# Kernel tuning notes

Hardware: AMD Instinct MI355X
Metric: run time of the kernel (lower is better)

Reference implementation:

```python
import jax, jax.numpy as jnp
import numpy as np

KERNEL_SIZE = 5
SIGMA = 2.0
HALF_K = KERNEL_SIZE // 2


def _gaussian_kernel():
    # torch: arange(-k//2+1, k//2+1) with python floor div -> [-2,...,2] for k=5
    ax = jnp.arange(-(KERNEL_SIZE // 2), KERNEL_SIZE // 2 + 1, dtype=jnp.float32)
    xx, yy = jnp.meshgrid(ax, ax, indexing='ij')
    k = jnp.exp(-(xx ** 2 + yy ** 2) / (2.0 * SIGMA ** 2))
    return k / k.sum()  # [5,5]


def setup_inputs() -> dict:
    key = jax.random.key(0)
    k1, k2 = jax.random.split(key)
    feature_map = jax.random.normal(k1, (512, 256, 256), dtype=jnp.float32)
    keypoints = jax.random.randint(k2, (4096, 2), 0, 256, dtype=jnp.int64)
    return {"feature_map": feature_map, "keypoints": keypoints}


def reference(feature_map, keypoints):
    C, H, W = feature_map.shape
    kern = _gaussian_kernel().astype(feature_map.dtype)  # [5,5]
    x = jnp.clip(keypoints[:, 0].astype(jnp.int32), HALF_K, W - HALF_K - 1)  # [N]
    y = jnp.clip(keypoints[:, 1].astype(jnp.int32), HALF_K, H - HALF_K - 1)  # [N]

    def pool_one(xi, yi):
        patch = jax.lax.dynamic_slice(
            feature_map, (0, yi - HALF_K, xi - HALF_K), (C, KERNEL_SIZE, KERNEL_SIZE)
        )  # [C,5,5]
        return jnp.einsum('chw,hw->c', patch, kern)  # [C]

    return jax.vmap(pool_one)(x, y)  # [N,C]
```

## Files before the change

kernel.cpp:

```cpp
#include <hip/hip_runtime.h>


#define NC  512
#define NH  256
#define NW  256
#define NKP 4096

#define NSTRIP 16
#define SLICE_ROWS 20
#define STR 260

#define WS_LIST_OFF_I 8192

__global__ __launch_bounds__(256) void bucket_kernel(
    const int* __restrict__ kp, unsigned* __restrict__ ws_i, int n_kp)
{
    __shared__ int hist[NSTRIP];
    __shared__ int base[NSTRIP];
    const int t = threadIdx.x;
    const int i = blockIdx.x * 256 + t;

    if (t < NSTRIP) hist[t] = 0;
    __syncthreads();

    int q = 0, lr = 0;
    unsigned pk = 0;
    const bool valid = (i < n_kp);
    if (valid) {
        int x = kp[2 * i + 0];
        int y = kp[2 * i + 1];
        x = min(max(x, 2), NW - 3);
        y = min(max(y, 2), NH - 3);
        q  = y >> 4;
        lr = atomicAdd(&hist[q], 1);
        pk = (unsigned)i | ((unsigned)x << 12) | ((unsigned)y << 20);
    }
    __syncthreads();

    if (t < NSTRIP) base[t] = atomicAdd((int*)&ws_i[t], hist[t]);
    __syncthreads();

    if (valid)
        ws_i[WS_LIST_OFF_I + q * NKP + base[q] + lr] = pk;
}

__global__ __launch_bounds__(256) void pool_kernel(
    const float* __restrict__ fm, const unsigned* __restrict__ ws_i,
    float* __restrict__ out)
{
    __shared__ float plane[SLICE_ROWS * STR];

    const int b     = blockIdx.x;
    const int x7    = b & 7;
    const int inner = b >> 3;
    const int hi    = inner >> 8;
    const int rem   = inner & 255;
    const int q     = rem >> 4;
    const int lane  = rem & 15;
    const int chunk = (hi << 3) | x7;
    const int c     = (chunk << 4) | lane;

    const int t = threadIdx.x;
    const int ybase = (q << 4) - 2;

    const float4* src = (const float4*)(fm + ((size_t)c << 16));
#pragma unroll
    for (int it = 0; it < 5; ++it) {
        const int i = t + it * 256;
        const int row  = i >> 6;
        const int col4 = i & 63;
        const int gr   = ybase + row;
        if ((unsigned)gr < 256u) {
            float4 v = src[(gr << 6) + col4];
            *(float4*)&plane[row * STR + (col4 << 2)] = v;
        }
    }
    __syncthreads();

    const float e1 = 0.8824969025845955f;
    const float e2 = 0.6065306597126334f;
    const float s  = 2.0f * (e1 + e2) + 1.0f;
    const float inv_s2 = 1.0f / (s * s);
    const float g[5] = {e2, e1, 1.0f, e1, e2};
    float gy[5];
#pragma unroll
    for (int i = 0; i < 5; i++) gy[i] = g[i] * inv_s2;

    const int cnt = (int)ws_i[q];
    const unsigned* list = ws_i + WS_LIST_OFF_I + q * NKP;

    for (int e = t; e < cnt; e += 256) {
        const unsigned pk = list[e];
        const int n  = (int)(pk & 0xFFFu);
        const int xc = (int)((pk >> 12) & 0xFFu);
        const int yc = (int)((pk >> 20) & 0xFFu);

        const int x0 = xc - 2;
        const int r  = x0 & 3;
        const int xa = x0 - r;
        float wx[8];
#pragma unroll
        for (int i = 0; i < 8; i++)
            wx[i] = (i >= r && i < r + 5) ? g[i - r] : 0.0f;

        const int lr0 = yc - (q << 4);
        float acc = 0.0f;
#pragma unroll
        for (int dy = 0; dy < 5; dy++) {
            const float* rowp = &plane[(lr0 + dy) * STR + xa];
            float4 a = *(const float4*)rowp;
            float4 b4 = *(const float4*)(rowp + 4);
            acc += gy[dy] * (a.x * wx[0] + a.y * wx[1] + a.z * wx[2] + a.w * wx[3]
                           + b4.x * wx[4] + b4.y * wx[5] + b4.z * wx[6] + b4.w * wx[7]);
        }
        out[(size_t)n * NC + c] = acc;
    }
}

__global__ __launch_bounds__(256) void gpool_direct_kernel(
    const float* __restrict__ fm, const int* __restrict__ kp,
    float* __restrict__ out)
{
    const int n = blockIdx.x;
    const int t = threadIdx.x;

    int x = kp[2 * n + 0];
    int y = kp[2 * n + 1];
    x = min(max(x, 2), NW - 3);
    y = min(max(y, 2), NH - 3);

    const float e1 = 0.8824969025845955f;
    const float e2 = 0.6065306597126334f;
    const float s  = 2.0f * (e1 + e2) + 1.0f;
    const float inv_s2 = 1.0f / (s * s);
    float g[5] = {e2, e1, 1.0f, e1, e2};
    float gy[5];
#pragma unroll
    for (int i = 0; i < 5; i++) gy[i] = g[i] * inv_s2;

    const int x0 = x - 2;
    const int r  = x0 & 3;
    const int xa = x0 - r;
    float wx[8];
#pragma unroll
    for (int i = 0; i < 8; i++)
        wx[i] = (i >= r && i < r + 5) ? g[i - r] : 0.0f;

    const float* base0 = fm + ((size_t)t * NH + (y - 2)) * NW + xa;
    const float* base1 = fm + ((size_t)(t + 256) * NH + (y - 2)) * NW + xa;

    float acc0 = 0.0f, acc1 = 0.0f;
#pragma unroll
    for (int dy = 0; dy < 5; dy++) {
        const float4* p0 = (const float4*)(base0 + dy * NW);
        const float4* p1 = (const float4*)(base1 + dy * NW);
        float4 a0 = p0[0], b0 = p0[1], a1 = p1[0], b1 = p1[1];
        acc0 += gy[dy] * (a0.x * wx[0] + a0.y * wx[1] + a0.z * wx[2] + a0.w * wx[3]
                        + b0.x * wx[4] + b0.y * wx[5] + b0.z * wx[6] + b0.w * wx[7]);
        acc1 += gy[dy] * (a1.x * wx[0] + a1.y * wx[1] + a1.z * wx[2] + a1.w * wx[3]
                        + b1.x * wx[4] + b1.y * wx[5] + b1.z * wx[6] + b1.w * wx[7]);
    }

    out[(size_t)n * NC + t]       = acc0;
    out[(size_t)n * NC + t + 256] = acc1;
}

extern "C" void kernel_launch(void* const* d_in, const int* in_sizes, int n_in,
                              void* d_out, int out_size, void* d_ws, size_t ws_size,
                              hipStream_t stream)
{
    const float* fm  = (const float*)d_in[0];
    const int*   kp  = (const int*)d_in[1];
    float*       out = (float*)d_out;
    const int n_kp   = in_sizes[1] / 2;

    const size_t need = (WS_LIST_OFF_I + (size_t)NSTRIP * NKP) * sizeof(unsigned);
    if (ws_size >= need && n_kp == NKP) {
        unsigned* ws_i = (unsigned*)d_ws;

        hipMemsetAsync(d_ws, 0, NSTRIP * sizeof(unsigned), stream);

        bucket_kernel<<<(NKP + 255) / 256, 256, 0, stream>>>(kp, ws_i, n_kp);

        pool_kernel<<<NC * NSTRIP, 256, 0, stream>>>(fm, ws_i, out);
    } else {
        gpool_direct_kernel<<<n_kp, 256, 0, stream>>>(fm, kp, out);
    }
}
```

Before: 203.8 us.

## Use single-block bucketing and direct global-to-LDS loads for strip staging

The bucketing pass now runs in one 1024-thread block that writes counts directly. This removes the memset and the global atomics used to compute per-block bases. The pool kernel stages each feature-map strip into shared memory with global_load_lds (buffer-to-LDS DMA) instead of loading through registers, and it moves the count load and weight setup before the barrier so they overlap the transfer. The trade-offs are that bucketing is serialized onto a single CU and the code now depends on an AMD-specific builtin with 16-byte width support.

After: 200.6 us. About the same (-1.6%).

```diff
diff --git a/kernel.cpp b/kernel.cpp
--- a/kernel.cpp
+++ b/kernel.cpp
@@ -12,36 +12,41 @@
 
 #define WS_LIST_OFF_I 8192
 
-__global__ __launch_bounds__(256) void bucket_kernel(
+__global__ __launch_bounds__(1024) void bucket_kernel(
     const int* __restrict__ kp, unsigned* __restrict__ ws_i, int n_kp)
 {
     __shared__ int hist[NSTRIP];
-    __shared__ int base[NSTRIP];
     const int t = threadIdx.x;
-    const int i = blockIdx.x * 256 + t;
 
     if (t < NSTRIP) hist[t] = 0;
     __syncthreads();
 
-    int q = 0, lr = 0;
-    unsigned pk = 0;
-    const bool valid = (i < n_kp);
-    if (valid) {
-        int x = kp[2 * i + 0];
-        int y = kp[2 * i + 1];
-        x = min(max(x, 2), NW - 3);
-        y = min(max(y, 2), NH - 3);
-        q  = y >> 4;
-        lr = atomicAdd(&hist[q], 1);
-        pk = (unsigned)i | ((unsigned)x << 12) | ((unsigned)y << 20);
+    int      q[4], lr[4];
+    unsigned pk[4];
+    bool     valid[4];
+#pragma unroll
+    for (int j = 0; j < 4; ++j) {
+        const int i = t + j * 1024;
+        valid[j] = (i < n_kp);
+        q[j] = 0; lr[j] = 0; pk[j] = 0u;
+        if (valid[j]) {
+            int x = kp[2 * i + 0];
+            int y = kp[2 * i + 1];
+            x = min(max(x, 2), NW - 3);
+            y = min(max(y, 2), NH - 3);
+            q[j]  = y >> 4;
+            lr[j] = atomicAdd(&hist[q[j]], 1);
+            pk[j] = (unsigned)i | ((unsigned)x << 12) | ((unsigned)y << 20);
+        }
     }
     __syncthreads();
 
-    if (t < NSTRIP) base[t] = atomicAdd((int*)&ws_i[t], hist[t]);
-    __syncthreads();
+    if (t < NSTRIP) ws_i[t] = (unsigned)hist[t];
 
-    if (valid)
-        ws_i[WS_LIST_OFF_I + q * NKP + base[q] + lr] = pk;
+#pragma unroll
+    for (int j = 0; j < 4; ++j)
+        if (valid[j])
+            ws_i[WS_LIST_OFF_I + q[j] * NKP + lr[j]] = pk[j];
 }
 
 __global__ __launch_bounds__(256) void pool_kernel(
@@ -56,26 +61,31 @@
     const int hi    = inner >> 8;
     const int rem   = inner & 255;
     const int q     = rem >> 4;
-    const int lane  = rem & 15;
+    const int l16   = rem & 15;
     const int chunk = (hi << 3) | x7;
-    const int c     = (chunk << 4) | lane;
+    const int c     = (chunk << 4) | l16;
 
-    const int t = threadIdx.x;
+    const int t    = threadIdx.x;
+    const int w    = t >> 6;
+    const int lane = t & 63;
     const int ybase = (q << 4) - 2;
 
-    const float4* src = (const float4*)(fm + ((size_t)c << 16));
+    const int cnt = (int)ws_i[q];
+
+    const float* src = fm + ((size_t)c << 16);
 #pragma unroll
     for (int it = 0; it < 5; ++it) {
-        const int i = t + it * 256;
-        const int row  = i >> 6;
-        const int col4 = i & 63;
-        const int gr   = ybase + row;
+        const int row = w + (it << 2);
+        const int gr  = ybase + row;
         if ((unsigned)gr < 256u) {
-            float4 v = src[(gr << 6) + col4];
-            *(float4*)&plane[row * STR + (col4 << 2)] = v;
+            const float* g = src + ((size_t)gr << 8) + (lane << 2);
+            float*       l = &plane[row * STR + (lane << 2)];
+            __builtin_amdgcn_global_load_lds(
+                (const __attribute__((address_space(1))) void*)g,
+                (__attribute__((address_space(3))) void*)l,
+                16, 0, 0);
         }
     }
-    __syncthreads();
 
     const float e1 = 0.8824969025845955f;
     const float e2 = 0.6065306597126334f;
@@ -86,7 +96,8 @@
 #pragma unroll
     for (int i = 0; i < 5; i++) gy[i] = g[i] * inv_s2;
 
-    const int cnt = (int)ws_i[q];
+    __syncthreads();
+
     const unsigned* list = ws_i + WS_LIST_OFF_I + q * NKP;
 
     for (int e = t; e < cnt; e += 256) {
@@ -108,7 +119,7 @@
 #pragma unroll
         for (int dy = 0; dy < 5; dy++) {
             const float* rowp = &plane[(lr0 + dy) * STR + xa];
-            float4 a = *(const float4*)rowp;
+            float4 a  = *(const float4*)rowp;
             float4 b4 = *(const float4*)(rowp + 4);
             acc += gy[dy] * (a.x * wx[0] + a.y * wx[1] + a.z * wx[2] + a.w * wx[3]
                            + b4.x * wx[4] + b4.y * wx[5] + b4.z * wx[6] + b4.w * wx[7]);
@@ -178,9 +189,7 @@
     if (ws_size >= need && n_kp == NKP) {
         unsigned* ws_i = (unsigned*)d_ws;
 
-        hipMemsetAsync(d_ws, 0, NSTRIP * sizeof(unsigned), stream);
-
-        bucket_kernel<<<(NKP + 255) / 256, 256, 0, stream>>>(kp, ws_i, n_kp);
+        bucket_kernel<<<1, 1024, 0, stream>>>(kp, ws_i, n_kp);
 
         pool_kernel<<<NC * NSTRIP, 256, 0, stream>>>(fm, ws_i, out);
     } else {
```
